# Optimization experiments

Hardware: AMD Instinct MI355X
Metric: run time of the kernel (lower is better)

Reference implementation:

```python
import jax, jax.numpy as jnp
import numpy as np

B, T_IN, T_OUT, N, FEAT = 32, 96, 96, 512, 8
HID = 512
GRID_SIZE, SPLINE_ORDER = 5, 3
GRID_RANGE = (-1.0, 1.0)


def _make_grid():
    # matches KANLinear.create_grid: identical row per in_feature, so keep 1-D
    h = (GRID_RANGE[1] - GRID_RANGE[0]) / GRID_SIZE
    return jnp.arange(-SPLINE_ORDER, GRID_SIZE + SPLINE_ORDER + 1, dtype=jnp.float32) * h + GRID_RANGE[0]


def _b_splines(x, grid):
    # x: [M, in_features]; de Boor-Cox recursion, order SPLINE_ORDER
    x = x[..., None]  # [M, in, 1]
    bases = ((x >= grid[:-1]) & (x < grid[1:])).astype(x.dtype)
    for k in range(1, SPLINE_ORDER + 1):
        left = (x - grid[:-(k + 1)]) / (grid[k:-1] - grid[:-(k + 1)])
        right = (grid[k + 1:] - x) / (grid[k + 1:] - grid[1:-k])
        bases = left * bases[..., :-1] + right * bases[..., 1:]
    return bases  # [M, in, grid_size + spline_order]


def setup_inputs() -> dict:
    key = jax.random.key(0)
    ks = jax.random.split(key, 12)
    s = 0.05
    return {
        "X": jax.random.normal(ks[0], (B, T_IN, N, FEAT), jnp.float32),
        "Y": jax.random.normal(ks[1], (B, T_OUT, N, FEAT), jnp.float32),
        "Wx": jax.random.normal(ks[2], (HID, T_IN * FEAT), jnp.float32) * s,
        "bx": jax.random.normal(ks[3], (HID,), jnp.float32) * s,
        "Wy": jax.random.normal(ks[4], (HID, T_OUT * FEAT), jnp.float32) * s,
        "by": jax.random.normal(ks[5], (HID,), jnp.float32) * s,
        "base_w": jax.random.normal(ks[6], (64, 2 * HID), jnp.float32) * s,
        "spline_w": jax.random.normal(ks[7], (64, 2 * HID, GRID_SIZE + SPLINE_ORDER), jnp.float32) * s,
        "spline_scaler": jax.random.normal(ks[8], (64, 2 * HID), jnp.float32) * s,
        "Wf": jax.random.normal(ks[9], (T_OUT * FEAT, 64), jnp.float32) * s,
        "bf": jax.random.normal(ks[10], (T_OUT * FEAT,), jnp.float32) * s,
    }


def reference(X, Y, Wx, bx, Wy, by, base_w, spline_w, spline_scaler, Wf, bf):
    # [B, T, N, F] -> [B, N, T*F]
    Xf = jnp.transpose(X, (0, 2, 1, 3)).reshape(B, N, T_IN * FEAT)
    Yf = jnp.transpose(Y, (0, 2, 1, 3)).reshape(B, N, T_OUT * FEAT)
    Hx = jnp.tanh(Xf @ Wx.T + bx)
    Hy = jnp.tanh(Yf @ Wy.T + by)
    h = jnp.concatenate([Hx, Hy], axis=-1).reshape(B * N, 2 * HID)

    grid = _make_grid()
    base_out = jax.nn.silu(h) @ base_w.T
    scaled_sw = spline_w * spline_scaler[..., None]  # [out, in, coeff]
    spline_out = jnp.einsum("mik,oik->mo", _b_splines(h, grid), scaled_sw)
    kan_out = (base_out + spline_out).reshape(B, N, 64)

    out = kan_out @ Wf.T + bf  # [B, N, T_OUT*FEAT]
    out = out.reshape(B, N, T_OUT, FEAT)
    return jnp.transpose(out, (0, 2, 1, 3))  # [B, T_OUT, N, FEAT]
```

## Files before the change

### kernel.cpp

```cpp
#include <hip/hip_runtime.h>
#include <cmath>

#define B_    32
#define T_    96
#define N_    512
#define F_    8
#define TF_   768
#define HID_  512
#define M_    16384
#define KIN_  1024
#define KS_   4

typedef short short8 __attribute__((ext_vector_type(8)));
typedef float f32x4  __attribute__((ext_vector_type(4)));
typedef unsigned int  uintx4 __attribute__((ext_vector_type(4)));
typedef unsigned long long ulongx2 __attribute__((ext_vector_type(2)));
typedef unsigned short      ushort_t;
typedef unsigned int        uint_t;
typedef unsigned long long  ulong_t;

#define HT_B     0ull
#define WQ_B     33554432ull
#define WB_B     34734080ull
#define SH_B     36306944ull
#define KANR_B   61472768ull
#define WFQ_B    63569920ull

static __device__ inline uint_t  fbits(float f){ return __builtin_bit_cast(uint_t, f); }
static __device__ inline ushort_t f2b(float f){
    uint_t u = fbits(f);
    return (ushort_t)((u + 0x7fffu + ((u >> 16) & 1u)) >> 16);
}
static __device__ inline float b2f(ushort_t h){ return __builtin_bit_cast(float, (uint_t)h << 16); }
static __device__ inline ulong_t pack4(float4 v){
    return (ulong_t)f2b(v.x) | ((ulong_t)f2b(v.y) << 16) |
           ((ulong_t)f2b(v.z) << 32) | ((ulong_t)f2b(v.w) << 48);
}
static __device__ inline ulong_t pack4t(float4 v){
    uint_t d0 = (fbits(v.x) >> 16) | (fbits(v.y) & 0xffff0000u);
    uint_t d1 = (fbits(v.z) >> 16) | (fbits(v.w) & 0xffff0000u);
    return (ulong_t)d0 | ((ulong_t)d1 << 32);
}
static __device__ inline float fast_tanh(float x){
    const float e = __expf(2.0f * x);
    return 1.0f - 2.0f / (e + 1.0f);
}
static __device__ inline void gload_lds16(const void* g, void* l){
    __builtin_amdgcn_global_load_lds(
        (const __attribute__((address_space(1))) unsigned int*)g,
        (__attribute__((address_space(3))) unsigned int*)l, 16, 0, 0);
}

__global__ __launch_bounds__(256) void pack_wq4(
    const float* __restrict__ base_w,
    const float* __restrict__ spline_w,
    const float* __restrict__ scaler,
    ushort_t* __restrict__ wq)
{
    const int e = blockIdx.x * 256 + threadIdx.x;
    const int j    = e & 7;
    const int ln   = (e >> 3) & 63;
    const int ct   = (e >> 9) & 3;
    const int t    = (e >> 11) & 3;
    const int rest = e >> 13;
    const int ss   = rest % 18;
    const int ks   = rest / 18;
    const int o = ct * 16 + (ln & 15);
    const int g = ln >> 4;
    float v;
    if (ss < 16) {
        const int i = ks * 256 + ss * 16 + t * 4 + g;
        v = spline_w[(o * KIN_ + i) * 8 + j] * scaler[o * KIN_ + i];
    } else {
        const int i = ks * 256 + (ss - 16) * 128 + t * 32 + g * 8 + j;
        v = base_w[o * KIN_ + i];
    }
    wq[e] = f2b(v);
}

__global__ __launch_bounds__(256) void pack_wb2(
    const float* __restrict__ Wx,
    const float* __restrict__ Wy,
    ushort_t* __restrict__ wb)
{
    const int e = blockIdx.x * 256 + threadIdx.x;
    const float v = (e < 512 * TF_) ? Wx[e] : Wy[e - 512 * TF_];
    wb[e] = f2b(v);
}

__global__ __launch_bounds__(256) void pack_wfq(
    const float* __restrict__ Wf, ushort_t* __restrict__ wfq)
{
    const int e = blockIdx.x * 256 + threadIdx.x;
    const int jj  = e & 7;
    const int ln  = (e >> 3) & 63;
    const int rt  = (e >> 9) & 3;
    const int s   = (e >> 11) & 1;
    const int wvt = (e >> 12) & 1;
    const int tb  = e >> 13;
    const int tf = tb * 128 + wvt * 64 + rt * 16 + (ln & 15);
    const int o  = s * 32 + (ln >> 4) * 8 + jj;
    wfq[e] = f2b(Wf[(size_t)tf * 64 + o]);
}

__global__ __launch_bounds__(256) void xcvt_kernel(
    const float* __restrict__ Xs, ushort_t* __restrict__ xbf)
{
    __shared__ __align__(16) char lds[32 * 1552];
    const int tid = threadIdx.x;
    const int n0  = blockIdx.x * 32;
    const int bb  = blockIdx.y;
    const int nl  = (tid & 63) >> 1;
    const int f4  = (tid & 1) * 4;
    const int tq  = tid >> 6;
    #pragma unroll 4
    for (int u = 0; u < 24; u++) {
        const int t = u * 4 + tq;
        const float4 v = *(const float4*)(Xs + (size_t)bb * (T_ * N_ * F_)
                                             + (size_t)t * (N_ * F_)
                                             + (size_t)(n0 + nl) * F_ + f4);
        *(ulong_t*)(lds + nl * 1552 + t * 16 + f4 * 2) = pack4t(v);
    }
    __syncthreads();
    #pragma unroll 4
    for (int u = 0; u < 12; u++) {
        const int c   = u * 256 + tid;
        const int row = c / 96;
        const int col = c - row * 96;
        const uintx4 val = *(const uintx4*)(lds + row * 1552 + col * 16);
        *(uintx4*)(xbf + (size_t)(bb * 512 + n0 + row) * TF_ + col * 8) = val;
    }
}

__global__ __launch_bounds__(512, 2) void gemm_tanh_v7(
    const ushort_t* __restrict__ xbf,
    const ushort_t* __restrict__ wb,
    const float* __restrict__ bias,
    ushort_t* __restrict__ ht, int z)
{
    __shared__ __align__(16) char smem[32768];

    const int tid = threadIdx.x;
    const int wv  = tid >> 6;
    const int ln  = tid & 63;
    const int lr  = ln & 15;
    const int hi  = ln >> 4;
    const int wm  = wv >> 2;
    const int wj  = wv & 3;

    const int m0  = blockIdx.x * 128;
    const int jl0 = blockIdx.y * 128;
    const int j0  = z * 512 + jl0;

    const int r_l = ln >> 3;
    const int ck  = ((ln & 7) ^ r_l) * 8;

    f32x4 acc[4][2] = {};

    for (int kt = 0; kt < 12; kt++) {
        __syncthreads();
        #pragma unroll
        for (int s = 0; s < 2; s++) {
            const int reg = s * 8 + wv;
            const int row = reg * 8 + r_l;
            gload_lds16(xbf + (size_t)(m0 + row) * TF_ + kt * 64 + ck,
                        smem + reg * 1024 + ln * 16);
            gload_lds16(wb + (size_t)(j0 + row) * TF_ + kt * 64 + ck,
                        smem + 16384 + reg * 1024 + ln * 16);
        }
        __syncthreads();

        #pragma unroll
        for (int h = 0; h < 2; h++) {
            const int g = h * 4 + hi;
            short8 a[4], b[2];
            #pragma unroll
            for (int rt = 0; rt < 4; rt++) {
                const int r = wm * 64 + rt * 16 + lr;
                a[rt] = *(short8*)(smem + r * 128 + ((g ^ (r & 7)) * 16));
            }
            #pragma unroll
            for (int ct = 0; ct < 2; ct++) {
                const int r = wj * 32 + ct * 16 + lr;
                b[ct] = *(short8*)(smem + 16384 + r * 128 + ((g ^ (r & 7)) * 16));
            }
            #pragma unroll
            for (int rt = 0; rt < 4; rt++)
                #pragma unroll
                for (int ct = 0; ct < 2; ct++)
                    acc[rt][ct] = __builtin_amdgcn_mfma_f32_16x16x32_bf16(
                        a[rt], b[ct], acc[rt][ct], 0, 0, 0);
        }
    }

    __syncthreads();
    #pragma unroll
    for (int ct = 0; ct < 2; ct++) {
        const int j = wj * 32 + ct * 16 + lr;
        const float bvv = bias[jl0 + j];
        #pragma unroll
        for (int rt = 0; rt < 4; rt++) {
            const f32x4 v = acc[rt][ct];
            float4 tv;
            tv.x = fast_tanh(v[0] + bvv);
            tv.y = fast_tanh(v[1] + bvv);
            tv.z = fast_tanh(v[2] + bvv);
            tv.w = fast_tanh(v[3] + bvv);
            const int slot = wm * 8 + rt * 2 + (hi >> 1);
            *(ulong_t*)(smem + j * 256 + ((slot ^ (j & 15)) * 16) + (hi & 1) * 8)
                = pack4(tv);
        }
    }
    __syncthreads();
    {
        const int j  = tid >> 2;
        const int q4 = tid & 3;
        ushort_t* dst = ht + (size_t)(j0 + j) * M_ + m0 + q4 * 32;
        #pragma unroll
        for (int w = 0; w < 4; w++) {
            const int slot = q4 * 4 + w;
            short8 val = *(short8*)(smem + j * 256 + ((slot ^ (j & 15)) * 16));
            *(short8*)(dst + w * 8) = val;
        }
    }
}

static __device__ inline short8 eval_bases(float x)
{
    const float v = fmaf(x, 2.5f, 2.5f);
    float sf = floorf(v);
    sf = fminf(fmaxf(sf, 0.0f), 4.0f);
    const float u = v - sf;
    const int si = (int)sf;
    const float u2 = u * u, u3 = u2 * u;
    const float omu = 1.0f - u;
    const float omu3 = omu * omu * omu;
    const float Bb0 = omu3 * (1.0f / 6.0f);
    const float Bb3 = u3 * (1.0f / 6.0f);
    const float Bb1 = fmaf(0.5f, u3, 2.0f / 3.0f) - u2;
    const float Bb2 = 1.0f - Bb0 - Bb1 - Bb3;
    const uint_t d0 = (fbits(Bb0) >> 16) | (fbits(Bb1) & 0xffff0000u);
    const uint_t d1 = (fbits(Bb2) >> 16) | (fbits(Bb3) & 0xffff0000u);
    const ulong_t P = (ulong_t)d0 | ((ulong_t)d1 << 32);
    const int sh = si << 4;
    const ulong_t Plo = P << (sh & 63);
    const ulong_t Phi = P >> ((64 - sh) & 63);
    ulongx2 pr;
    pr.x = (si == 4) ? 0ull : Plo;
    pr.y = (si == 0) ? 0ull : ((si == 4) ? P : Phi);
    return __builtin_bit_cast(short8, pr);
}

static __device__ inline short8 eval_silu8(const ushort_t* __restrict__ ht, int ib0, size_t r)
{
    uintx4 d;
    #pragma unroll
    for (int jj = 0; jj < 4; jj++) {
        const float x0 = b2f(ht[(size_t)(ib0 + 2 * jj)     * M_ + r]);
        const float x1 = b2f(ht[(size_t)(ib0 + 2 * jj + 1) * M_ + r]);
        const float s0 = x0 / (1.0f + __expf(-x0));
        const float s1 = x1 / (1.0f + __expf(-x1));
        d[jj] = (fbits(s0) >> 16) | (fbits(s1) & 0xffff0000u);
    }
    return __builtin_bit_cast(short8, d);
}

__global__ __launch_bounds__(256) void kan_v4(
    const ushort_t* __restrict__ ht,
    const ushort_t* __restrict__ wq,
    float* __restrict__ kanp)
{
    const int tid = threadIdx.x;
    const int wv  = tid >> 6;
    const int ln  = tid & 63;
    const int g   = ln >> 4;
    const int lr  = ln & 15;
    const int m0  = blockIdx.x * 64;
    const int ks  = blockIdx.y;
    const int iB  = ks * 256;
    const size_t r0 = (size_t)(m0 + wv * 16 + lr);

    const short8* wqf = (const short8*)wq + (size_t)ks * 18432 + ln;

    f32x4 acc[4] = {};

    for (int ss = 0; ss < 16; ss++) {
        #pragma unroll
        for (int t = 0; t < 4; t++) {
            const short8* bp = wqf + (size_t)(ss * 4 + t) * 256;
            const short8 b0 = bp[0], b1 = bp[64], b2 = bp[128], b3 = bp[192];
            const int i = iB + ss * 16 + t * 4 + g;
            const short8 a0 = eval_bases(b2f(ht[(size_t)i * M_ + r0]));
            acc[0] = __builtin_amdgcn_mfma_f32_16x16x32_bf16(a0, b0, acc[0], 0, 0, 0);
            acc[1] = __builtin_amdgcn_mfma_f32_16x16x32_bf16(a0, b1, acc[1], 0, 0, 0);
            acc[2] = __builtin_amdgcn_mfma_f32_16x16x32_bf16(a0, b2, acc[2], 0, 0, 0);
            acc[3] = __builtin_amdgcn_mfma_f32_16x16x32_bf16(a0, b3, acc[3], 0, 0, 0);
        }
    }
    #pragma unroll
    for (int st = 0; st < 2; st++) {
        #pragma unroll
        for (int t = 0; t < 4; t++) {
            const short8* bp = wqf + (size_t)((16 + st) * 4 + t) * 256;
            const short8 b0 = bp[0], b1 = bp[64], b2 = bp[128], b3 = bp[192];
            const int ib0 = iB + st * 128 + t * 32 + g * 8;
            const short8 a0 = eval_silu8(ht, ib0, r0);
            acc[0] = __builtin_amdgcn_mfma_f32_16x16x32_bf16(a0, b0, acc[0], 0, 0, 0);
            acc[1] = __builtin_amdgcn_mfma_f32_16x16x32_bf16(a0, b1, acc[1], 0, 0, 0);
            acc[2] = __builtin_amdgcn_mfma_f32_16x16x32_bf16(a0, b2, acc[2], 0, 0, 0);
            acc[3] = __builtin_amdgcn_mfma_f32_16x16x32_bf16(a0, b3, acc[3], 0, 0, 0);
        }
    }

    #pragma unroll
    for (int ct = 0; ct < 4; ct++) {
        const int o = ct * 16 + lr;
        #pragma unroll
        for (int q = 0; q < 4; q++) {
            const size_t row = (size_t)(m0 + wv * 16 + (ln >> 4) * 4 + q);
            kanp[(size_t)ks * (M_ * 64) + row * 64 + o] = acc[ct][q];
        }
    }
}

__global__ __launch_bounds__(256) void reduce_kan(
    const float* __restrict__ kanp, ushort_t* __restrict__ kanr)
{
    const int e8 = blockIdx.x * 256 + threadIdx.x;
    const size_t base = (size_t)e8 * 8;
    float4 s0 = *(const float4*)(kanp + base);
    float4 s1 = *(const float4*)(kanp + base + 4);
    #pragma unroll
    for (int p = 1; p < KS_; p++) {
        const float4 a0 = *(const float4*)(kanp + (size_t)p * (M_ * 64) + base);
        const float4 a1 = *(const float4*)(kanp + (size_t)p * (M_ * 64) + base + 4);
        s0.x += a0.x; s0.y += a0.y; s0.z += a0.z; s0.w += a0.w;
        s1.x += a1.x; s1.y += a1.y; s1.z += a1.z; s1.w += a1.w;
    }
    ulongx2 outv;
    outv.x = pack4(s0);
    outv.y = pack4(s1);
    *(ulongx2*)(kanr + base) = outv;
}

__global__ __launch_bounds__(256) void final_v2(
    const ushort_t* __restrict__ kanr,
    const ushort_t* __restrict__ wfq,
    const float* __restrict__ bf,
    float* __restrict__ out)
{
    const int tid = threadIdx.x;
    const int wv  = tid >> 6;
    const int ln  = tid & 63;
    const int lr  = ln & 15;
    const int hi  = ln >> 4;
    const int wvm = wv >> 1;
    const int wvt = wv & 1;
    const int mb  = blockIdx.x;
    const int tb  = blockIdx.y;

    f32x4 acc[4][4] = {};

    #pragma unroll
    for (int s = 0; s < 2; s++) {
        short8 afr[4], bfr[4];
        #pragma unroll
        for (int rt = 0; rt < 4; rt++) {
            const size_t idx = ((size_t)(((tb * 2 + wvt) * 2 + s) * 4 + rt)) * 64 + ln;
            afr[rt] = ((const short8*)wfq)[idx];
        }
        #pragma unroll
        for (int ct = 0; ct < 4; ct++) {
            const int m = mb * 128 + wvm * 64 + ct * 16 + lr;
            bfr[ct] = *(const short8*)(kanr + (size_t)m * 64 + s * 32 + hi * 8);
        }
        #pragma unroll
        for (int rt = 0; rt < 4; rt++)
            #pragma unroll
            for (int ct = 0; ct < 4; ct++)
                acc[rt][ct] = __builtin_amdgcn_mfma_f32_16x16x32_bf16(
                    afr[rt], bfr[ct], acc[rt][ct], 0, 0, 0);
    }

    #pragma unroll
    for (int rt = 0; rt < 4; rt++) {
        const int tf0 = tb * 128 + wvt * 64 + rt * 16 + hi * 4;
        const float4 b4 = *(const float4*)&bf[tf0];
        const int t  = tf0 >> 3;
        const int f0 = tf0 & 7;
        #pragma unroll
        for (int ct = 0; ct < 4; ct++) {
            const int m = mb * 128 + wvm * 64 + ct * 16 + lr;
            const int bb = m >> 9;
            const int n  = m & 511;
            const f32x4 v = acc[rt][ct];
            float4 o4 = make_float4(v[0] + b4.x, v[1] + b4.y, v[2] + b4.z, v[3] + b4.w);
            *(float4*)&out[(size_t)bb * (T_ * N_ * F_)
                           + (size_t)t * (N_ * F_)
                           + (size_t)n * F_ + f0] = o4;
        }
    }
}

extern "C" void kernel_launch(void* const* d_in, const int* in_sizes, int n_in,
                              void* d_out, int out_size, void* d_ws, size_t ws_size,
                              hipStream_t stream)
{
    const float* X      = (const float*)d_in[0];
    const float* Y      = (const float*)d_in[1];
    const float* Wx     = (const float*)d_in[2];
    const float* bx     = (const float*)d_in[3];
    const float* Wy     = (const float*)d_in[4];
    const float* by     = (const float*)d_in[5];
    const float* base_w = (const float*)d_in[6];
    const float* spline_w = (const float*)d_in[7];
    const float* spline_scaler = (const float*)d_in[8];
    const float* Wf     = (const float*)d_in[9];
    const float* bf     = (const float*)d_in[10];

    float* out = (float*)d_out;
    ushort_t* ht   = (ushort_t*)((char*)d_ws + HT_B);
    ushort_t* wq   = (ushort_t*)((char*)d_ws + WQ_B);
    ushort_t* wb   = (ushort_t*)((char*)d_ws + WB_B);
    ushort_t* xbf  = (ushort_t*)((char*)d_ws + SH_B);
    float*    kanp = (float*)((char*)d_ws + SH_B);
    ushort_t* kanr = (ushort_t*)((char*)d_ws + KANR_B);
    ushort_t* wfq  = (ushort_t*)((char*)d_ws + WFQ_B);

    pack_wq4<<<2304, 256, 0, stream>>>(base_w, spline_w, spline_scaler, wq);
    pack_wb2<<<3072, 256, 0, stream>>>(Wx, Wy, wb);
    pack_wfq<<<192, 256, 0, stream>>>(Wf, wfq);

    xcvt_kernel<<<dim3(16, 32), 256, 0, stream>>>(X, xbf);
    gemm_tanh_v7<<<dim3(128, 4), 512, 0, stream>>>(xbf, wb, bx, ht, 0);
    xcvt_kernel<<<dim3(16, 32), 256, 0, stream>>>(Y, xbf);
    gemm_tanh_v7<<<dim3(128, 4), 512, 0, stream>>>(xbf, wb, by, ht, 1);

    kan_v4<<<dim3(M_ / 64, KS_), 256, 0, stream>>>(ht, wq, kanp);
    reduce_kan<<<512, 256, 0, stream>>>(kanp, kanr);
    final_v2<<<dim3(128, 6), 256, 0, stream>>>(kanr, wfq, bf, out);
}
```

Baseline: 146.4 us.

## Double KAN split-K to eight slices and store partials in fp16

New measurement: 144.6 us. Within noise of the previous version (-1.2%).

```diff
diff --git a/kernel.cpp b/kernel.cpp
--- a/kernel.cpp
+++ b/kernel.cpp
@@ -9,12 +9,13 @@
 #define HID_  512
 #define M_    16384
 #define KIN_  1024
-#define KS_   4
+#define KS_   8
 
 typedef short short8 __attribute__((ext_vector_type(8)));
 typedef float f32x4  __attribute__((ext_vector_type(4)));
 typedef unsigned int  uintx4 __attribute__((ext_vector_type(4)));
 typedef unsigned long long ulongx2 __attribute__((ext_vector_type(2)));
+typedef _Float16 halfx8 __attribute__((ext_vector_type(8)));
 typedef unsigned short      ushort_t;
 typedef unsigned int        uint_t;
 typedef unsigned long long  ulong_t;
@@ -51,7 +52,7 @@
         (__attribute__((address_space(3))) unsigned int*)l, 16, 0, 0);
 }
 
-__global__ __launch_bounds__(256) void pack_wq4(
+__global__ __launch_bounds__(256) void pack_wq(
     const float* __restrict__ base_w,
     const float* __restrict__ spline_w,
     const float* __restrict__ scaler,
@@ -63,16 +64,16 @@
     const int ct   = (e >> 9) & 3;
     const int t    = (e >> 11) & 3;
     const int rest = e >> 13;
-    const int ss   = rest % 18;
-    const int ks   = rest / 18;
+    const int ss   = rest % 9;
+    const int ks   = rest / 9;
     const int o = ct * 16 + (ln & 15);
     const int g = ln >> 4;
     float v;
-    if (ss < 16) {
-        const int i = ks * 256 + ss * 16 + t * 4 + g;
+    if (ss < 8) {
+        const int i = ks * 128 + ss * 16 + t * 4 + g;
         v = spline_w[(o * KIN_ + i) * 8 + j] * scaler[o * KIN_ + i];
     } else {
-        const int i = ks * 256 + (ss - 16) * 128 + t * 32 + g * 8 + j;
+        const int i = ks * 128 + t * 32 + g * 8 + j;
         v = base_w[o * KIN_ + i];
     }
     wq[e] = f2b(v);
@@ -251,24 +252,10 @@
     return __builtin_bit_cast(short8, pr);
 }
 
-static __device__ inline short8 eval_silu8(const ushort_t* __restrict__ ht, int ib0, size_t r)
-{
-    uintx4 d;
-    #pragma unroll
-    for (int jj = 0; jj < 4; jj++) {
-        const float x0 = b2f(ht[(size_t)(ib0 + 2 * jj)     * M_ + r]);
-        const float x1 = b2f(ht[(size_t)(ib0 + 2 * jj + 1) * M_ + r]);
-        const float s0 = x0 / (1.0f + __expf(-x0));
-        const float s1 = x1 / (1.0f + __expf(-x1));
-        d[jj] = (fbits(s0) >> 16) | (fbits(s1) & 0xffff0000u);
-    }
-    return __builtin_bit_cast(short8, d);
-}
-
-__global__ __launch_bounds__(256) void kan_v4(
+__global__ __launch_bounds__(256) void kan_v5(
     const ushort_t* __restrict__ ht,
     const ushort_t* __restrict__ wq,
-    float* __restrict__ kanp)
+    _Float16* __restrict__ kanp)
 {
     const int tid = threadIdx.x;
     const int wv  = tid >> 6;
@@ -277,20 +264,21 @@
     const int lr  = ln & 15;
     const int m0  = blockIdx.x * 64;
     const int ks  = blockIdx.y;
-    const int iB  = ks * 256;
+    const int iB  = ks * 128;
     const size_t r0 = (size_t)(m0 + wv * 16 + lr);
 
-    const short8* wqf = (const short8*)wq + (size_t)ks * 18432 + ln;
+    const short8* wqf = (const short8*)wq + (size_t)ks * 9216 + ln;
+    const ushort_t* htg  = ht + (size_t)(iB + g) * M_ + r0;
+    const ushort_t* htg8 = ht + (size_t)(iB + g * 8) * M_ + r0;
 
     f32x4 acc[4] = {};
 
-    for (int ss = 0; ss < 16; ss++) {
+    for (int ss = 0; ss < 8; ss++) {
         #pragma unroll
         for (int t = 0; t < 4; t++) {
             const short8* bp = wqf + (size_t)(ss * 4 + t) * 256;
             const short8 b0 = bp[0], b1 = bp[64], b2 = bp[128], b3 = bp[192];
-            const int i = iB + ss * 16 + t * 4 + g;
-            const short8 a0 = eval_bases(b2f(ht[(size_t)i * M_ + r0]));
+            const short8 a0 = eval_bases(b2f(htg[(size_t)(ss * 16 + t * 4) * M_]));
             acc[0] = __builtin_amdgcn_mfma_f32_16x16x32_bf16(a0, b0, acc[0], 0, 0, 0);
             acc[1] = __builtin_amdgcn_mfma_f32_16x16x32_bf16(a0, b1, acc[1], 0, 0, 0);
             acc[2] = __builtin_amdgcn_mfma_f32_16x16x32_bf16(a0, b2, acc[2], 0, 0, 0);
@@ -298,18 +286,23 @@
         }
     }
     #pragma unroll
-    for (int st = 0; st < 2; st++) {
-        #pragma unroll
-        for (int t = 0; t < 4; t++) {
-            const short8* bp = wqf + (size_t)((16 + st) * 4 + t) * 256;
-            const short8 b0 = bp[0], b1 = bp[64], b2 = bp[128], b3 = bp[192];
-            const int ib0 = iB + st * 128 + t * 32 + g * 8;
-            const short8 a0 = eval_silu8(ht, ib0, r0);
-            acc[0] = __builtin_amdgcn_mfma_f32_16x16x32_bf16(a0, b0, acc[0], 0, 0, 0);
-            acc[1] = __builtin_amdgcn_mfma_f32_16x16x32_bf16(a0, b1, acc[1], 0, 0, 0);
-            acc[2] = __builtin_amdgcn_mfma_f32_16x16x32_bf16(a0, b2, acc[2], 0, 0, 0);
-            acc[3] = __builtin_amdgcn_mfma_f32_16x16x32_bf16(a0, b3, acc[3], 0, 0, 0);
-        }
+    for (int t = 0; t < 4; t++) {
+        const short8* bp = wqf + (size_t)(32 + t) * 256;
+        const short8 b0 = bp[0], b1 = bp[64], b2 = bp[128], b3 = bp[192];
+        uintx4 d;
+        #pragma unroll
+        for (int jj = 0; jj < 4; jj++) {
+            const float x0 = b2f(htg8[(size_t)(t * 32 + 2 * jj)     * M_]);
+            const float x1 = b2f(htg8[(size_t)(t * 32 + 2 * jj + 1) * M_]);
+            const float s0 = x0 / (1.0f + __expf(-x0));
+            const float s1 = x1 / (1.0f + __expf(-x1));
+            d[jj] = (fbits(s0) >> 16) | (fbits(s1) & 0xffff0000u);
+        }
+        const short8 a0 = __builtin_bit_cast(short8, d);
+        acc[0] = __builtin_amdgcn_mfma_f32_16x16x32_bf16(a0, b0, acc[0], 0, 0, 0);
+        acc[1] = __builtin_amdgcn_mfma_f32_16x16x32_bf16(a0, b1, acc[1], 0, 0, 0);
+        acc[2] = __builtin_amdgcn_mfma_f32_16x16x32_bf16(a0, b2, acc[2], 0, 0, 0);
+        acc[3] = __builtin_amdgcn_mfma_f32_16x16x32_bf16(a0, b3, acc[3], 0, 0, 0);
     }
 
     #pragma unroll
@@ -317,26 +310,26 @@
         const int o = ct * 16 + lr;
         #pragma unroll
         for (int q = 0; q < 4; q++) {
-            const size_t row = (size_t)(m0 + wv * 16 + (ln >> 4) * 4 + q);
-            kanp[(size_t)ks * (M_ * 64) + row * 64 + o] = acc[ct][q];
+            const size_t row = (size_t)(m0 + wv * 16 + g * 4 + q);
+            kanp[(size_t)ks * (M_ * 64) + row * 64 + o] = (_Float16)acc[ct][q];
         }
     }
 }
 
 __global__ __launch_bounds__(256) void reduce_kan(
-    const float* __restrict__ kanp, ushort_t* __restrict__ kanr)
+    const _Float16* __restrict__ kanp, ushort_t* __restrict__ kanr)
 {
     const int e8 = blockIdx.x * 256 + threadIdx.x;
     const size_t base = (size_t)e8 * 8;
-    float4 s0 = *(const float4*)(kanp + base);
-    float4 s1 = *(const float4*)(kanp + base + 4);
-    #pragma unroll
-    for (int p = 1; p < KS_; p++) {
-        const float4 a0 = *(const float4*)(kanp + (size_t)p * (M_ * 64) + base);
-        const float4 a1 = *(const float4*)(kanp + (size_t)p * (M_ * 64) + base + 4);
-        s0.x += a0.x; s0.y += a0.y; s0.z += a0.z; s0.w += a0.w;
-        s1.x += a1.x; s1.y += a1.y; s1.z += a1.z; s1.w += a1.w;
-    }
+    float s[8] = {};
+    #pragma unroll
+    for (int p = 0; p < KS_; p++) {
+        const halfx8 v = *(const halfx8*)(kanp + (size_t)p * (M_ * 64) + base);
+        #pragma unroll
+        for (int j = 0; j < 8; j++) s[j] += (float)v[j];
+    }
+    float4 s0 = make_float4(s[0], s[1], s[2], s[3]);
+    float4 s1 = make_float4(s[4], s[5], s[6], s[7]);
     ulongx2 outv;
     outv.x = pack4(s0);
     outv.y = pack4(s1);
@@ -423,11 +416,11 @@
     ushort_t* wq   = (ushort_t*)((char*)d_ws + WQ_B);
     ushort_t* wb   = (ushort_t*)((char*)d_ws + WB_B);
     ushort_t* xbf  = (ushort_t*)((char*)d_ws + SH_B);
-    float*    kanp = (float*)((char*)d_ws + SH_B);
+    _Float16* kanp = (_Float16*)((char*)d_ws + SH_B);
     ushort_t* kanr = (ushort_t*)((char*)d_ws + KANR_B);
     ushort_t* wfq  = (ushort_t*)((char*)d_ws + WFQ_B);
 
-    pack_wq4<<<2304, 256, 0, stream>>>(base_w, spline_w, spline_scaler, wq);
+    pack_wq<<<2304, 256, 0, stream>>>(base_w, spline_w, spline_scaler, wq);
     pack_wb2<<<3072, 256, 0, stream>>>(Wx, Wy, wb);
     pack_wfq<<<192, 256, 0, stream>>>(Wf, wfq);
 
@@ -436,7 +429,7 @@
     xcvt_kernel<<<dim3(16, 32), 256, 0, stream>>>(Y, xbf);
     gemm_tanh_v7<<<dim3(128, 4), 512, 0, stream>>>(xbf, wb, by, ht, 1);
 
-    kan_v4<<<dim3(M_ / 64, KS_), 256, 0, stream>>>(ht, wq, kanp);
+    kan_v5<<<dim3(M_ / 64, KS_), 256, 0, stream>>>(ht, wq, kanp);
     reduce_kan<<<512, 256, 0, stream>>>(kanp, kanr);
     final_v2<<<dim3(128, 6), 256, 0, stream>>>(kanr, wfq, bf, out);
 }
```
